# Performance work log

Hardware: AMD Instinct MI355X
Metric: run time of the kernel (lower is better)

The kernel has to match this reference:

```python
import jax, jax.numpy as jnp
import numpy as np

N_NODE = 4096   # nodes per graph (generalized from hardcoded 55)
IN_DIM = 200    # input_dim, forced by attn1 in_channel=200
OUT_DIM = 200   # output_dim, forced equal to input_dim by GRU_gate shapes
N_HEADS = 8     # forced by attn2 in_channel 1600 = 8*200
SEQ_LEN = 4
HID = 200       # hid_units default


def _glorot(k, shape):
    r = np.sqrt(6.0 / (shape[0] + shape[1])).astype(np.float32)
    return jax.random.uniform(k, shape, jnp.float32, -r, r)


def setup_inputs() -> dict:
    key = jax.random.key(0)
    ks = jax.random.split(key, 32)
    inp = {}
    mask = jax.random.bernoulli(ks[0], 0.01, (SEQ_LEN, N_NODE, N_NODE))
    inp['adjs'] = jax.random.uniform(ks[1], (SEQ_LEN, N_NODE, N_NODE), jnp.float32) * mask
    inp['feats'] = jax.random.normal(ks[2], (SEQ_LEN, N_NODE, IN_DIM), jnp.float32)
    inp['p_covss'] = jnp.zeros((SEQ_LEN,), jnp.float32)  # passed but unused in original
    # per-head weight_vars, randn(output_dim, input_dim) in original call()
    inp['init_wv'] = jax.random.normal(ks[3], (N_HEADS, OUT_DIM, IN_DIM), jnp.float32)
    # attn1 (shared across all heads): conv1d(k=1) == linear
    inp['W1'] = _glorot(ks[4], (HID, IN_DIM)); inp['b1'] = jnp.zeros((HID,), jnp.float32)
    inp['a11'] = _glorot(ks[5], (HID, 1))[:, 0]; inp['a11b'] = jnp.zeros((), jnp.float32)
    inp['a12'] = _glorot(ks[6], (HID, 1))[:, 0]; inp['a12b'] = jnp.zeros((), jnp.float32)
    # attn2
    inp['W2'] = _glorot(ks[7], (OUT_DIM, N_HEADS * HID)); inp['b2'] = jnp.zeros((OUT_DIM,), jnp.float32)
    inp['a21'] = _glorot(ks[8], (OUT_DIM, 1))[:, 0]; inp['a21b'] = jnp.zeros((), jnp.float32)
    inp['a22'] = _glorot(ks[9], (OUT_DIM, 1))[:, 0]; inp['a22b'] = jnp.zeros((), jnp.float32)
    # GRU gates (reset/update/htilda), reduce=True since n_node != input_dim
    for i, g in enumerate(['r', 'u', 'h']):
        inp['W' + g] = _glorot(ks[10 + 4 * i], (N_NODE, OUT_DIM))
        inp['U' + g] = _glorot(ks[11 + 4 * i], (OUT_DIM, OUT_DIM))
        inp['P' + g] = _glorot(ks[12 + 4 * i], (IN_DIM, N_NODE))
        inp['b' + g] = jnp.zeros((IN_DIM, OUT_DIM), jnp.float32)
    return inp


def reference(adjs, feats, p_covss, init_wv, W1, b1, a11, a11b, a12, a12b,
              W2, b2, a21, a21b, a22, a22b,
              Wr, Ur, Pr, br, Wu, Uu, Pu, bu, Wh, Uh, Ph, bh):
    def gat(x):  # x: [N, IN_DIM]
        fts = x @ W1.T + b1                                   # [N, HID]
        # logits f_1 + f_2^T on [N,1,1] stays [N,1,1]; softmax over the
        # singleton dim is identically 1 -> attention is degenerate.
        s = jax.nn.leaky_relu((fts @ a11 + a11b) + (fts @ a12 + a12b), 0.01)
        coefs = jnp.ones_like(s)                              # softmax([N,1,1], dim=1)
        h = jax.nn.elu(coefs[:, None] * fts)                  # [N, HID]
        hcat = jnp.tile(h, (1, N_HEADS))                      # heads share attn1 -> identical
        fts2 = hcat @ W2.T + b2                               # [N, OUT_DIM]
        s2 = jax.nn.leaky_relu((fts2 @ a21 + a21b) + (fts2 @ a22 + a22b), 0.01)
        coefs2 = jnp.ones_like(s2)
        out = jax.nn.elu(coefs2[:, None] * fts2)              # [N, OUT_DIM]
        # torch: out.view(nb_classes, -1).T then softmax(dim=1), then view(-1, out_dim)
        logits = jnp.reshape(out, (OUT_DIM, N_NODE)).T        # memory reinterpretation, not transpose
        return jax.nn.softmax(logits, axis=1)                 # [N, OUT_DIM]

    embeds = jax.vmap(gat)(feats)                             # [T, N, OUT_DIM]

    def gru_step(wv, adj):  # wv: [H, OUT_DIM, IN_DIM=OUT_DIM], adj: [N, N]
        # head-independent sparse propagation bases, one per gate
        gr = Pr @ (adj @ Wr) + br                             # [IN_DIM, OUT_DIM]
        gu = Pu @ (adj @ Wu) + bu
        gh = Ph @ (adj @ Wh) + bh
        r = jax.nn.sigmoid(gr + wv @ Ur)                      # [H, 200, 200]
        u = jax.nn.sigmoid(gu + wv @ Uu)
        hcap = jnp.tanh(gh + (r * wv) @ Uh)
        return (1.0 - u) * wv + u * hcap, None

    final_wv, _ = jax.lax.scan(gru_step, init_wv, adjs[1:])   # evolve over t=1..T-1
    return embeds, final_wv
```

## Files before the change

kernel.cpp:

```cpp
#include <hip/hip_runtime.h>
#include <hip/hip_bf16.h>
#include <math.h>

typedef __hip_bfloat16 bf16;
typedef __attribute__((ext_vector_type(8))) short short8;
typedef __attribute__((ext_vector_type(4))) float f32x4;

#define N_NODE 4096
#define DIM 200
#define NH 8
#define SEQ 4
#define TLDA 40

__device__ __forceinline__ float eluf(float x) { return x > 0.f ? x : expm1f(x); }
__device__ __forceinline__ float sigm(float x) { return 1.f / (1.f + expf(-x)); }

template<bool ISB>
__device__ __forceinline__ float ldv(const void* p, size_t i) {
    if (ISB) return __bfloat162float(((const bf16*)p)[i]);
    else     return ((const float*)p)[i];
}
template<bool ISB>
__device__ __forceinline__ void stv(void* p, size_t i, float v) {
    if (ISB) ((bf16*)p)[i] = __float2bfloat16(v);
    else     ((float*)p)[i] = v;
}
__device__ __forceinline__ float bflo(unsigned u) { return __uint_as_float((u & 0xffffu) << 16); }
__device__ __forceinline__ float bfhi(unsigned u) { return __uint_as_float(u & 0xffff0000u); }
__device__ __forceinline__ short f2bs(float v) {
    bf16 h = __float2bfloat16(v);
    return *(short*)&h;
}

__global__ void k_detect(const void* feats, int* flag) {
    __shared__ int cnt;
    if (threadIdx.x == 0) cnt = 0;
    __syncthreads();
    const unsigned short* u = (const unsigned short*)feats;
    unsigned short v = u[2 * threadIdx.x];
    int e = (v >> 7) & 0xFF;
    if (e >= 100 && e <= 140) atomicAdd(&cnt, 1);
    __syncthreads();
    if (threadIdx.x == 0) *flag = (cnt >= 128) ? 1 : 0;
}


template<bool AISB>
__device__ __forceinline__ void ldA8(const void* A, int lda, int arow, bool rowOK,
                                     int kk, int K, float* la) {
    if (rowOK && kk + 8 <= K) {
        if (AISB) {
            const unsigned short* ap = (const unsigned short*)A + (size_t)arow * lda + kk;
            uint4 u = *(const uint4*)ap;
            la[0] = bflo(u.x); la[1] = bfhi(u.x);
            la[2] = bflo(u.y); la[3] = bfhi(u.y);
            la[4] = bflo(u.z); la[5] = bfhi(u.z);
            la[6] = bflo(u.w); la[7] = bfhi(u.w);
        } else {
            const float* ap = (const float*)A + (size_t)arow * lda + kk;
            float4 f0 = *(const float4*)ap;
            float4 f1 = *(const float4*)(ap + 4);
            la[0] = f0.x; la[1] = f0.y; la[2] = f0.z; la[3] = f0.w;
            la[4] = f1.x; la[5] = f1.y; la[6] = f1.z; la[7] = f1.w;
        }
    } else {
#pragma unroll
        for (int j = 0; j < 8; j++)
            la[j] = (rowOK && kk + j < K) ? ldv<AISB>(A, (size_t)arow * lda + kk + j) : 0.f;
    }
}
template<bool BISB>
__device__ __forceinline__ void ldB8(const void* B, int gcol, bool colOK,
                                     int kk, int K, float* lb) {
#pragma unroll
    for (int j = 0; j < 8; j++)
        lb[j] = (colOK && kk + j < K) ? ldv<BISB>(B, (size_t)(kk + j) * DIM + gcol) : 0.f;
}

template<int EPI, bool AISB, bool BISB>
__device__ void mgemm(const void* A, int lda, const void* B, int M, int K,
                      int kbeg, int kend, const float* X1, const float* X2,
                      float* C, int row0, int c0, const int* fl, void* out2) {
    const int N = DIM;
    int tid = threadIdx.x;
    int wave = tid >> 6, lane = tid & 63;
    int m16 = lane & 15, q = lane >> 4;
    __shared__ short As[64 * TLDA];
    __shared__ short Bs[64 * TLDA];
    int s_row = tid >> 2;
    int s_k   = (tid & 3) * 8;
    int b_col = tid & 63;
    int b_kg  = (tid >> 6) * 8;
    int arow = row0 + s_row;
    bool rowOK = arow < M;
    int gcol = c0 + b_col;
    bool colOK = gcol < N;
    float la[8], lb[8];
    ldA8<AISB>(A, lda, arow, rowOK, kbeg + s_k, K, la);
    ldB8<BISB>(B, gcol, colOK, kbeg + b_kg, K, lb);
    f32x4 acc[4] = {};
    for (int k0 = kbeg; k0 < kend; k0 += 32) {
        __syncthreads();
        short8 a8, b8;
#pragma unroll
        for (int j = 0; j < 8; j++) { a8[j] = f2bs(la[j]); b8[j] = f2bs(lb[j]); }
        *(short8*)&As[s_row * TLDA + s_k] = a8;
        *(short8*)&Bs[b_col * TLDA + b_kg] = b8;
        __syncthreads();
        int kn = k0 + 32;
        if (kn < kend) {
            ldA8<AISB>(A, lda, arow, rowOK, kn + s_k, K, la);
            ldB8<BISB>(B, gcol, colOK, kn + b_kg, K, lb);
        }
        short8 bf = *(short8*)&Bs[(wave * 16 + m16) * TLDA + q * 8];
#pragma unroll
        for (int r = 0; r < 4; r++) {
            short8 af = *(short8*)&As[(r * 16 + m16) * TLDA + q * 8];
            acc[r] = __builtin_amdgcn_mfma_f32_16x16x32_bf16(af, bf, acc[r], 0, 0, 0);
        }
    }
    int colw = c0 + wave * 16 + m16;
    if (colw >= N) return;
#pragma unroll
    for (int r = 0; r < 4; r++) {
        int rowb = row0 + r * 16 + q * 4;
#pragma unroll
        for (int reg = 0; reg < 4; reg++) {
            int row = rowb + reg;
            if (row >= M) continue;
            float v = acc[r][reg];
            size_t ci = (size_t)row * 200 + colw;
            if (EPI == 0) {
                C[ci] = eluf(v + X1[colw]);
            } else if (EPI == 3) {
                int a200 = row - (row / 200) * 200;
                float uu = X2[ci];
                float hc = tanhf(X1[a200 * 200 + colw] + v);
                float nv = (1.f - uu) * C[ci] + uu * hc;
                C[ci] = nv;
                if (out2) {
                    size_t oo = (size_t)SEQ * N_NODE * DIM + ci;
                    if (*fl) stv<true>(out2, oo, nv); else stv<false>(out2, oo, nv);
                }
            } else {
                atomicAdd(&C[ci], v);
            }
        }
    }
}

__global__ __launch_bounds__(256) void k_gemm_e12(const float* A,
        const float* Br, const float* Bu, const float* Gr, const float* Gu,
        float* rw, float* u) {
    const int M = NH * DIM, K = DIM, N = DIM;
    int row0 = blockIdx.y * 64, c0 = blockIdx.x * 64;
    int tid = threadIdx.x;
    int wave = tid >> 6, lane = tid & 63;
    int m16 = lane & 15, q = lane >> 4;
    __shared__ short As[64 * TLDA];
    __shared__ short Bsr[64 * TLDA];
    __shared__ short Bsu[64 * TLDA];
    int s_row = tid >> 2;
    int s_k   = (tid & 3) * 8;
    int b_col = tid & 63;
    int b_kg  = (tid >> 6) * 8;
    int arow = row0 + s_row;
    bool rowOK = arow < M;
    int gcol = c0 + b_col;
    bool colOK = gcol < N;
    float la[8], lbr[8], lbu[8];
    ldA8<false>(A, K, arow, rowOK, s_k, K, la);
    ldB8<false>(Br, gcol, colOK, b_kg, K, lbr);
    ldB8<false>(Bu, gcol, colOK, b_kg, K, lbu);
    f32x4 accR[4] = {}, accU[4] = {};
    for (int k0 = 0; k0 < K; k0 += 32) {
        __syncthreads();
        short8 a8, r8, u8;
#pragma unroll
        for (int j = 0; j < 8; j++) {
            a8[j] = f2bs(la[j]); r8[j] = f2bs(lbr[j]); u8[j] = f2bs(lbu[j]);
        }
        *(short8*)&As[s_row * TLDA + s_k] = a8;
        *(short8*)&Bsr[b_col * TLDA + b_kg] = r8;
        *(short8*)&Bsu[b_col * TLDA + b_kg] = u8;
        __syncthreads();
        int kn = k0 + 32;
        if (kn < K) {
            ldA8<false>(A, K, arow, rowOK, kn + s_k, K, la);
            ldB8<false>(Br, gcol, colOK, kn + b_kg, K, lbr);
            ldB8<false>(Bu, gcol, colOK, kn + b_kg, K, lbu);
        }
        short8 bfr = *(short8*)&Bsr[(wave * 16 + m16) * TLDA + q * 8];
        short8 bfu = *(short8*)&Bsu[(wave * 16 + m16) * TLDA + q * 8];
#pragma unroll
        for (int r = 0; r < 4; r++) {
            short8 af = *(short8*)&As[(r * 16 + m16) * TLDA + q * 8];
            accR[r] = __builtin_amdgcn_mfma_f32_16x16x32_bf16(af, bfr, accR[r], 0, 0, 0);
            accU[r] = __builtin_amdgcn_mfma_f32_16x16x32_bf16(af, bfu, accU[r], 0, 0, 0);
        }
    }
    int colw = c0 + wave * 16 + m16;
    if (colw >= N) return;
#pragma unroll
    for (int r = 0; r < 4; r++) {
        int rowb = row0 + r * 16 + q * 4;
#pragma unroll
        for (int reg = 0; reg < 4; reg++) {
            int row = rowb + reg;
            if (row >= M) continue;
            int a200 = row - (row / 200) * 200;
            size_t ci = (size_t)row * 200 + colw;
            rw[ci] = sigm(Gr[a200 * 200 + colw] + accR[r][reg]) * A[ci];
            u[ci]  = sigm(Gu[a200 * 200 + colw] + accU[r][reg]);
        }
    }
}

__global__ __launch_bounds__(256) void k_gemm_e0(const int* fl, int useIsb,
        const void* A, int lda, const float* B, int M, int K,
        const float* bias, float* C) {
    int row0 = blockIdx.y * 64, c0 = blockIdx.x * 64;
    if (useIsb && *fl)
        mgemm<0, true , false>(A, lda, B, M, K, 0, K, bias, nullptr, C, row0, c0, nullptr, nullptr);
    else
        mgemm<0, false, false>(A, lda, B, M, K, 0, K, bias, nullptr, C, row0, c0, nullptr, nullptr);
}
__global__ __launch_bounds__(256) void k_gemm_e3(const float* A, const float* B,
        const float* G0, const float* U, float* WV, const int* fl, void* out2) {
    mgemm<3, false, false>(A, DIM, B, NH * DIM, DIM, 0, DIM, G0, U, WV,
                           blockIdx.y * 64, blockIdx.x * 64, fl, out2);
}
__global__ __launch_bounds__(256) void k_pggemm(const int* fl,
        const void* P0, const void* P1, const void* P2,
        const bf16* AWb, float* G) {
    int z = blockIdx.z;
    int sg = z >> 3, split = z & 7;
    int g = sg - (sg / 3) * 3;
    const void* A = (g == 0) ? P0 : (g == 1) ? P1 : P2;
    const void* B = AWb + (size_t)sg * N_NODE * DIM;
    float* C = G + (size_t)sg * DIM * DIM;
    int row0 = blockIdx.y * 64, c0 = blockIdx.x * 64;
    int kbeg = split * (N_NODE / 8), kend = kbeg + N_NODE / 8;
    if (*fl) mgemm<4, true , true>(A, N_NODE, B, DIM, N_NODE, kbeg, kend, nullptr, nullptr, C, row0, c0, nullptr, nullptr);
    else     mgemm<4, false, true>(A, N_NODE, B, DIM, N_NODE, kbeg, kend, nullptr, nullptr, C, row0, c0, nullptr, nullptr);
}

template<bool ISB>
__device__ void prep_body(const void* W1, const void* b1, const void* W2, const void* b2,
                          const void* Ur, const void* Uu, const void* Uh,
                          const void* br, const void* bu, const void* bh,
                          const void* iwv, const void* Wr, const void* Wu, const void* Wh,
                          float* W1t, float* W2t, float* b1f, float* b2f,
                          float* Utf, float* wv, float* G, unsigned short* Wcat) {
    int idx = blockIdx.x * 256 + threadIdx.x;
    if (idx < 40000) {
        int k = idx / 200, n = idx % 200;
        W1t[idx] = ldv<ISB>(W1, (size_t)n * 200 + k);
    } else if (idx < 80000) {
        int r = idx - 40000;
        int k = r / 200, n = r % 200;
        float s = 0.f;
        for (int h = 0; h < NH; h++) s += ldv<ISB>(W2, (size_t)n * 1600 + h * 200 + k);
        W2t[r] = s;
    } else if (idx < 80512) {
        int j = idx - 80000;
        if (j < 256)      b1f[j] = (j < 200) ? ldv<ISB>(b1, j) : 0.f;
        else              b2f[j - 256] = (j - 256 < 200) ? ldv<ISB>(b2, j - 256) : 0.f;
    } else if (idx < 200512) {
        int j = idx - 80512;
        int g = j / 40000, r = j - g * 40000;
        const void* U = (g == 0) ? Ur : (g == 1) ? Uu : Uh;
        Utf[j] = ldv<ISB>(U, r);
    } else if (idx < 520512) {
        wv[idx - 200512] = ldv<ISB>(iwv, idx - 200512);
    } else if (idx < 880512) {
        int j = idx - 520512;
        int sg = j / 40000, r = j - sg * 40000;
        int g = sg - (sg / 3) * 3;
        const void* bb = (g == 0) ? br : (g == 1) ? bu : bh;
        G[j] = ldv<ISB>(bb, r);
    } else {
        int j = idx - 880512;
        if (j < 4096 * 600) {
            int k = j / 600, c = j - k * 600;
            int g = (c < 200) ? 0 : (c < 400 ? 1 : 2);
            int o = c - g * 200;
            const void* W = (g == 0) ? Wr : (g == 1) ? Wu : Wh;
            bf16 v = __float2bfloat16(ldv<ISB>(W, (size_t)k * 200 + o));
            Wcat[(size_t)k * 608 + c] = *(unsigned short*)&v;
        }
    }
}
__global__ void k_prep(const int* fl, const void* W1, const void* b1, const void* W2,
                       const void* b2, const void* Ur, const void* Uu, const void* Uh,
                       const void* br, const void* bu, const void* bh, const void* iwv,
                       const void* Wr, const void* Wu, const void* Wh,
                       float* W1t, float* W2t, float* b1f, float* b2f,
                       float* Utf, float* wv, float* G, unsigned short* Wcat) {
    if (*fl) prep_body<true >(W1, b1, W2, b2, Ur, Uu, Uh, br, bu, bh, iwv, Wr, Wu, Wh,
                              W1t, W2t, b1f, b2f, Utf, wv, G, Wcat);
    else     prep_body<false>(W1, b1, W2, b2, Ur, Uu, Uh, br, bu, bh, iwv, Wr, Wu, Wh,
                              W1t, W2t, b1f, b2f, Utf, wv, G, Wcat);
}

template<bool ISB>
__device__ void softmax_body(const float* O, void* out) {
    __shared__ float tile[200 * 65];
    __shared__ float pm[4 * 64];
    __shared__ float ps[4 * 64];
    __shared__ float sm_m[64];
    __shared__ float sm_inv[64];
    int t = blockIdx.y;
    int i0 = blockIdx.x * 64;
    const float* ob = O + (size_t)t * N_NODE * DIM;
    int tid = threadIdx.x;
    for (int idx = tid; idx < 200 * 64; idx += 256) {
        int j = idx >> 6, c = idx & 63;
        tile[j * 65 + c] = ob[(size_t)j * N_NODE + i0 + c];
    }
    __syncthreads();
    int g = tid >> 6, lane = tid & 63;
    int j0 = g * 50, j1 = j0 + 50;
    float mp = -1e30f;
    for (int j = j0; j < j1; j++) mp = fmaxf(mp, tile[j * 65 + lane]);
    pm[g * 64 + lane] = mp;
    __syncthreads();
    if (tid < 64)
        sm_m[tid] = fmaxf(fmaxf(pm[tid], pm[64 + tid]), fmaxf(pm[128 + tid], pm[192 + tid]));
    __syncthreads();
    float mv = sm_m[lane];
    float sp = 0.f;
    for (int j = j0; j < j1; j++) {
        float e = expf(tile[j * 65 + lane] - mv);
        tile[j * 65 + lane] = e;
        sp += e;
    }
    ps[g * 64 + lane] = sp;
    __syncthreads();
    if (tid < 64)
        sm_inv[tid] = 1.f / (ps[tid] + ps[64 + tid] + ps[128 + tid] + ps[192 + tid]);
    __syncthreads();
    size_t ob2 = ((size_t)t * N_NODE + i0) * DIM;
    for (int idx = tid; idx < 64 * 200; idx += 256) {
        int il = idx / 200, j = idx - il * 200;
        stv<ISB>(out, ob2 + (size_t)il * DIM + j, tile[j * 65 + il] * sm_inv[il]);
    }
}
__global__ __launch_bounds__(256) void k_softmax(const int* fl, const float* O, void* out) {
    if (*fl) softmax_body<true>(O, out); else softmax_body<false>(O, out);
}

template<bool ISB>
__device__ void aw_body(const void* adjs, const unsigned short* Wcat, bf16* AWb) {
    int i = blockIdx.x;
    int s = blockIdx.y;
    size_t arow = ((size_t)(s + 1) * N_NODE + i) * N_NODE;
    __shared__ int   s_k[512];
    __shared__ float s_v[512];
    __shared__ int   s_cnt;
    int tid = threadIdx.x;
    if (tid == 0) s_cnt = 0;
    __syncthreads();
    float vals[16];
#pragma unroll
    for (int c = 0; c < 4; c++) {
        int col = c * 1024 + tid * 4;
        if (ISB) {
            ushort4 u = *(const ushort4*)((const unsigned short*)adjs + arow + col);
            vals[c*4+0] = __uint_as_float((unsigned)u.x << 16);
            vals[c*4+1] = __uint_as_float((unsigned)u.y << 16);
            vals[c*4+2] = __uint_as_float((unsigned)u.z << 16);
            vals[c*4+3] = __uint_as_float((unsigned)u.w << 16);
        } else {
            float4 f = *(const float4*)((const float*)adjs + arow + col);
            vals[c*4+0] = f.x; vals[c*4+1] = f.y; vals[c*4+2] = f.z; vals[c*4+3] = f.w;
        }
    }
#pragma unroll
    for (int q = 0; q < 16; q++) {
        if (vals[q] != 0.f) {
            int p = atomicAdd(&s_cnt, 1);
            if (p < 512) { s_k[p] = (q >> 2) * 1024 + tid * 4 + (q & 3); s_v[p] = vals[q]; }
        }
    }
    __syncthreads();
    int n = s_cnt < 512 ? s_cnt : 512;
    float a0 = 0.f, a1 = 0.f, d0 = 0.f, d1 = 0.f;
    bool hasB = (tid < 44);
    int offA = 2 * tid, offB = 512 + 2 * tid;
    int e = 0;
    for (; e + 4 <= n; e += 4) {
        int   k0 = s_k[e],   k1 = s_k[e+1], k2 = s_k[e+2], k3 = s_k[e+3];
        float v0 = s_v[e],   v1 = s_v[e+1], v2 = s_v[e+2], v3 = s_v[e+3];
        unsigned wa0 = *(const unsigned*)(Wcat + (size_t)k0 * 608 + offA);
        unsigned wa1 = *(const unsigned*)(Wcat + (size_t)k1 * 608 + offA);
        unsigned wa2 = *(const unsigned*)(Wcat + (size_t)k2 * 608 + offA);
        unsigned wa3 = *(const unsigned*)(Wcat + (size_t)k3 * 608 + offA);
        if (hasB) {
            unsigned wb0 = *(const unsigned*)(Wcat + (size_t)k0 * 608 + offB);
            unsigned wb1 = *(const unsigned*)(Wcat + (size_t)k1 * 608 + offB);
            unsigned wb2 = *(const unsigned*)(Wcat + (size_t)k2 * 608 + offB);
            unsigned wb3 = *(const unsigned*)(Wcat + (size_t)k3 * 608 + offB);
            d0 += v0*bflo(wb0) + v1*bflo(wb1) + v2*bflo(wb2) + v3*bflo(wb3);
            d1 += v0*bfhi(wb0) + v1*bfhi(wb1) + v2*bfhi(wb2) + v3*bfhi(wb3);
        }
        a0 += v0*bflo(wa0) + v1*bflo(wa1) + v2*bflo(wa2) + v3*bflo(wa3);
        a1 += v0*bfhi(wa0) + v1*bfhi(wa1) + v2*bfhi(wa2) + v3*bfhi(wa3);
    }
    for (; e < n; e++) {
        int k = s_k[e]; float v = s_v[e];
        unsigned wa = *(const unsigned*)(Wcat + (size_t)k * 608 + offA);
        a0 += v * bflo(wa); a1 += v * bfhi(wa);
        if (hasB) {
            unsigned wb = *(const unsigned*)(Wcat + (size_t)k * 608 + offB);
            d0 += v * bflo(wb); d1 += v * bfhi(wb);
        }
    }
    int gA = (offA < 200) ? 0 : (offA < 400 ? 1 : 2);
    int oA = offA - gA * 200;
    size_t wbase = ((size_t)(s * 3 + gA) * N_NODE + i) * DIM + oA;
    AWb[wbase]     = __float2bfloat16(a0);
    AWb[wbase + 1] = __float2bfloat16(a1);
    if (hasB) {
        int oB = offB - 400;
        size_t wb2 = ((size_t)(s * 3 + 2) * N_NODE + i) * DIM + oB;
        AWb[wb2]     = __float2bfloat16(d0);
        AWb[wb2 + 1] = __float2bfloat16(d1);
    }
}
__global__ __launch_bounds__(256) void k_aw(const int* fl, const void* adjs,
        const unsigned short* Wcat, bf16* AWb) {
    if (*fl) aw_body<true>(adjs, Wcat, AWb);
    else     aw_body<false>(adjs, Wcat, AWb);
}

extern "C" void kernel_launch(void* const* d_in, const int* in_sizes, int n_in,
                              void* d_out, int out_size, void* d_ws, size_t ws_size,
                              hipStream_t stream) {
    const void* adjs    = d_in[0];
    const void* feats   = d_in[1];
    const void* init_wv = d_in[3];
    const void* W1 = d_in[4];
    const void* b1 = d_in[5];
    const void* W2 = d_in[10];
    const void* b2 = d_in[11];
    const void* Wr = d_in[16];
    const void* Ur = d_in[17];
    const void* Pr = d_in[18];
    const void* br = d_in[19];
    const void* Wu = d_in[20];
    const void* Uu = d_in[21];
    const void* Pu = d_in[22];
    const void* bu = d_in[23];
    const void* Wh = d_in[24];
    const void* Uh = d_in[25];
    const void* Ph = d_in[26];
    const void* bh = d_in[27];

    int*   flag = (int*)d_ws;
    float* base = (float*)d_ws;
    unsigned short* Wcat = (unsigned short*)(base + 64);
    bf16*  AWb  = (bf16*)(base + 64 + 1245184);
    float* Hbuf = base + 64;
    float* Obuf = Hbuf + 3276800;
    float* W1t  = base + 6553664;
    float* W2t  = W1t + 40000;
    float* b1f  = W2t + 40000;
    float* b2f  = b1f + 256;
    float* ubuf = b2f + 256;
    float* rwbuf= ubuf + 320000;
    float* Utf  = rwbuf + 320000;
    float* G    = Utf + 120000;
    float* wv   = G + 360000;

    const int M = SEQ * N_NODE;

    k_detect<<<1, 256, 0, stream>>>(feats, flag);
    k_prep<<<(3338112 + 255) / 256, 256, 0, stream>>>(
        flag, W1, b1, W2, b2, Ur, Uu, Uh, br, bu, bh, init_wv, Wr, Wu, Wh,
        W1t, W2t, b1f, b2f, Utf, wv, G, Wcat);

    {
        dim3 g(N_NODE, 3);
        k_aw<<<g, 256, 0, stream>>>(flag, adjs, Wcat, AWb);
    }
    {
        dim3 g(4, 4, 72);
        k_pggemm<<<g, 256, 0, stream>>>(flag, Pr, Pu, Ph, AWb, G);
    }

    {
        dim3 g(4, M / 64);
        k_gemm_e0<<<g, 256, 0, stream>>>(flag, 1, feats, DIM, W1t, M, DIM, b1f, Hbuf);
        k_gemm_e0<<<g, 256, 0, stream>>>(flag, 0, Hbuf, DIM, W2t, M, DIM, b2f, Obuf);
    }
    {
        dim3 g(N_NODE / 64, SEQ);
        k_softmax<<<g, 256, 0, stream>>>(flag, Obuf, d_out);
    }

    {
        dim3 g(4, NH * DIM / 64);
        for (int s = 0; s < 3; s++) {
            const float* Gr = G + (size_t)(s * 3 + 0) * DIM * DIM;
            const float* Gu = G + (size_t)(s * 3 + 1) * DIM * DIM;
            const float* Gh = G + (size_t)(s * 3 + 2) * DIM * DIM;
            void* out2 = (s == 2) ? d_out : nullptr;
            k_gemm_e12<<<g, 256, 0, stream>>>(wv, Utf + 0, Utf + 40000, Gr, Gu, rwbuf, ubuf);
            k_gemm_e3<<<g, 256, 0, stream>>>(rwbuf, Utf + 80000, Gh, ubuf, wv, flag, out2);
        }
    }
}
```

Measured before the change: 671.3 us.

## Store GEMM operands in bf16 with transposed B for vectorized loads

Intermediate activations (H buffer, rw, wv copy) and the dense weights (W1, W2, U) are now kept in bf16. The weights are pre-transposed in the prep kernel so the B operand loads become single 16-byte vector loads instead of eight strided scalar loads. The per-iteration float-to-bf16 conversion in the GEMM loops is removed, and memory traffic for the intermediates roughly halves. In exchange the code keeps an extra bf16 copy of wv and adds conversion stores in the epilogues. The accuracy should match the previous path, since operands were already rounded to bf16 before the MFMA.

Result: faster. 595.3 us, median of 2 (-11.3%).

```diff
diff --git a/kernel.cpp b/kernel.cpp
--- a/kernel.cpp
+++ b/kernel.cpp
@@ -45,42 +45,55 @@
 }
 
 
-template<bool AISB>
-__device__ __forceinline__ void ldA8(const void* A, int lda, int arow, bool rowOK,
-                                     int kk, int K, float* la) {
+template<int AMODE>
+__device__ __forceinline__ short8 ldA8x(const void* A, int lda, int arow, bool rowOK,
+                                        int kk, int K) {
+    short8 r;
     if (rowOK && kk + 8 <= K) {
-        if (AISB) {
-            const unsigned short* ap = (const unsigned short*)A + (size_t)arow * lda + kk;
-            uint4 u = *(const uint4*)ap;
-            la[0] = bflo(u.x); la[1] = bfhi(u.x);
-            la[2] = bflo(u.y); la[3] = bfhi(u.y);
-            la[4] = bflo(u.z); la[5] = bfhi(u.z);
-            la[6] = bflo(u.w); la[7] = bfhi(u.w);
+        if (AMODE == 1) {
+            r = *(const short8*)((const short*)A + (size_t)arow * lda + kk);
         } else {
             const float* ap = (const float*)A + (size_t)arow * lda + kk;
             float4 f0 = *(const float4*)ap;
             float4 f1 = *(const float4*)(ap + 4);
-            la[0] = f0.x; la[1] = f0.y; la[2] = f0.z; la[3] = f0.w;
-            la[4] = f1.x; la[5] = f1.y; la[6] = f1.z; la[7] = f1.w;
+            r[0] = f2bs(f0.x); r[1] = f2bs(f0.y); r[2] = f2bs(f0.z); r[3] = f2bs(f0.w);
+            r[4] = f2bs(f1.x); r[5] = f2bs(f1.y); r[6] = f2bs(f1.z); r[7] = f2bs(f1.w);
         }
     } else {
 #pragma unroll
+        for (int j = 0; j < 8; j++) {
+            bool ok = rowOK && kk + j < K;
+            if (AMODE == 1) r[j] = ok ? ((const short*)A)[(size_t)arow * lda + kk + j] : (short)0;
+            else            r[j] = ok ? f2bs(((const float*)A)[(size_t)arow * lda + kk + j]) : (short)0;
+        }
+    }
+    return r;
+}
+
+template<int BMODE>
+__device__ __forceinline__ short8 ldB8x(const void* B, int gcol, bool colOK,
+                                        int kk, int K) {
+    short8 r;
+    if (BMODE == 2) {
+        if (colOK && kk + 8 <= K) {
+            r = *(const short8*)((const short*)B + (size_t)gcol * K + kk);
+        } else {
+#pragma unroll
+            for (int j = 0; j < 8; j++)
+                r[j] = (colOK && kk + j < K) ? ((const short*)B)[(size_t)gcol * K + kk + j] : (short)0;
+        }
+    } else {
+#pragma unroll
         for (int j = 0; j < 8; j++)
-            la[j] = (rowOK && kk + j < K) ? ldv<AISB>(A, (size_t)arow * lda + kk + j) : 0.f;
-    }
-}
-template<bool BISB>
-__device__ __forceinline__ void ldB8(const void* B, int gcol, bool colOK,
-                                     int kk, int K, float* lb) {
-#pragma unroll
-    for (int j = 0; j < 8; j++)
-        lb[j] = (colOK && kk + j < K) ? ldv<BISB>(B, (size_t)(kk + j) * DIM + gcol) : 0.f;
-}
-
-template<int EPI, bool AISB, bool BISB>
+            r[j] = (colOK && kk + j < K) ? ((const short*)B)[(size_t)(kk + j) * DIM + gcol] : (short)0;
+    }
+    return r;
+}
+
+template<int EPI, int AMODE, int BMODE, int CB16>
 __device__ void mgemm(const void* A, int lda, const void* B, int M, int K,
                       int kbeg, int kend, const float* X1, const float* X2,
-                      float* C, int row0, int c0, const int* fl, void* out2) {
+                      void* Cv, int row0, int c0, const int* fl, void* out2, short* Cb) {
     const int N = DIM;
     int tid = threadIdx.x;
     int wave = tid >> 6, lane = tid & 63;
@@ -95,28 +108,24 @@
     bool rowOK = arow < M;
     int gcol = c0 + b_col;
     bool colOK = gcol < N;
-    float la[8], lb[8];
-    ldA8<AISB>(A, lda, arow, rowOK, kbeg + s_k, K, la);
-    ldB8<BISB>(B, gcol, colOK, kbeg + b_kg, K, lb);
+    short8 la = ldA8x<AMODE>(A, lda, arow, rowOK, kbeg + s_k, K);
+    short8 lb = ldB8x<BMODE>(B, gcol, colOK, kbeg + b_kg, K);
     f32x4 acc[4] = {};
     for (int k0 = kbeg; k0 < kend; k0 += 32) {
         __syncthreads();
-        short8 a8, b8;
-#pragma unroll
-        for (int j = 0; j < 8; j++) { a8[j] = f2bs(la[j]); b8[j] = f2bs(lb[j]); }
-        *(short8*)&As[s_row * TLDA + s_k] = a8;
-        *(short8*)&Bs[b_col * TLDA + b_kg] = b8;
+        *(short8*)&As[s_row * TLDA + s_k] = la;
+        *(short8*)&Bs[b_col * TLDA + b_kg] = lb;
         __syncthreads();
         int kn = k0 + 32;
         if (kn < kend) {
-            ldA8<AISB>(A, lda, arow, rowOK, kn + s_k, K, la);
-            ldB8<BISB>(B, gcol, colOK, kn + b_kg, K, lb);
-        }
-        short8 bf = *(short8*)&Bs[(wave * 16 + m16) * TLDA + q * 8];
+            la = ldA8x<AMODE>(A, lda, arow, rowOK, kn + s_k, K);
+            lb = ldB8x<BMODE>(B, gcol, colOK, kn + b_kg, K);
+        }
+        short8 bfr = *(short8*)&Bs[(wave * 16 + m16) * TLDA + q * 8];
 #pragma unroll
         for (int r = 0; r < 4; r++) {
             short8 af = *(short8*)&As[(r * 16 + m16) * TLDA + q * 8];
-            acc[r] = __builtin_amdgcn_mfma_f32_16x16x32_bf16(af, bf, acc[r], 0, 0, 0);
+            acc[r] = __builtin_amdgcn_mfma_f32_16x16x32_bf16(af, bfr, acc[r], 0, 0, 0);
         }
     }
     int colw = c0 + wave * 16 + m16;
@@ -131,27 +140,31 @@
             float v = acc[r][reg];
             size_t ci = (size_t)row * 200 + colw;
             if (EPI == 0) {
-                C[ci] = eluf(v + X1[colw]);
+                float o = eluf(v + X1[colw]);
+                if (CB16) ((short*)Cv)[ci] = f2bs(o);
+                else      ((float*)Cv)[ci] = o;
             } else if (EPI == 3) {
+                float* C = (float*)Cv;
                 int a200 = row - (row / 200) * 200;
                 float uu = X2[ci];
                 float hc = tanhf(X1[a200 * 200 + colw] + v);
                 float nv = (1.f - uu) * C[ci] + uu * hc;
                 C[ci] = nv;
+                Cb[ci] = f2bs(nv);
                 if (out2) {
                     size_t oo = (size_t)SEQ * N_NODE * DIM + ci;
                     if (*fl) stv<true>(out2, oo, nv); else stv<false>(out2, oo, nv);
                 }
             } else {
-                atomicAdd(&C[ci], v);
+                atomicAdd(&((float*)Cv)[ci], v);
             }
         }
     }
 }
 
-__global__ __launch_bounds__(256) void k_gemm_e12(const float* A,
-        const float* Br, const float* Bu, const float* Gr, const float* Gu,
-        float* rw, float* u) {
+__global__ __launch_bounds__(256) void k_gemm_e12(const short* A,
+        const short* Br, const short* Bu, const float* Gr, const float* Gu,
+        const float* wvf, short* rwb, float* u) {
     const int M = NH * DIM, K = DIM, N = DIM;
     int row0 = blockIdx.y * 64, c0 = blockIdx.x * 64;
     int tid = threadIdx.x;
@@ -168,27 +181,21 @@
     bool rowOK = arow < M;
     int gcol = c0 + b_col;
     bool colOK = gcol < N;
-    float la[8], lbr[8], lbu[8];
-    ldA8<false>(A, K, arow, rowOK, s_k, K, la);
-    ldB8<false>(Br, gcol, colOK, b_kg, K, lbr);
-    ldB8<false>(Bu, gcol, colOK, b_kg, K, lbu);
+    short8 la = ldA8x<1>(A, K, arow, rowOK, s_k, K);
+    short8 lr = ldB8x<2>(Br, gcol, colOK, b_kg, K);
+    short8 lu = ldB8x<2>(Bu, gcol, colOK, b_kg, K);
     f32x4 accR[4] = {}, accU[4] = {};
     for (int k0 = 0; k0 < K; k0 += 32) {
         __syncthreads();
-        short8 a8, r8, u8;
-#pragma unroll
-        for (int j = 0; j < 8; j++) {
-            a8[j] = f2bs(la[j]); r8[j] = f2bs(lbr[j]); u8[j] = f2bs(lbu[j]);
-        }
-        *(short8*)&As[s_row * TLDA + s_k] = a8;
-        *(short8*)&Bsr[b_col * TLDA + b_kg] = r8;
-        *(short8*)&Bsu[b_col * TLDA + b_kg] = u8;
+        *(short8*)&As[s_row * TLDA + s_k] = la;
+        *(short8*)&Bsr[b_col * TLDA + b_kg] = lr;
+        *(short8*)&Bsu[b_col * TLDA + b_kg] = lu;
         __syncthreads();
         int kn = k0 + 32;
         if (kn < K) {
-            ldA8<false>(A, K, arow, rowOK, kn + s_k, K, la);
-            ldB8<false>(Br, gcol, colOK, kn + b_kg, K, lbr);
-            ldB8<false>(Bu, gcol, colOK, kn + b_kg, K, lbu);
+            la = ldA8x<1>(A, K, arow, rowOK, kn + s_k, K);
+            lr = ldB8x<2>(Br, gcol, colOK, kn + b_kg, K);
+            lu = ldB8x<2>(Bu, gcol, colOK, kn + b_kg, K);
         }
         short8 bfr = *(short8*)&Bsr[(wave * 16 + m16) * TLDA + q * 8];
         short8 bfu = *(short8*)&Bsu[(wave * 16 + m16) * TLDA + q * 8];
@@ -210,25 +217,31 @@
             if (row >= M) continue;
             int a200 = row - (row / 200) * 200;
             size_t ci = (size_t)row * 200 + colw;
-            rw[ci] = sigm(Gr[a200 * 200 + colw] + accR[r][reg]) * A[ci];
-            u[ci]  = sigm(Gu[a200 * 200 + colw] + accU[r][reg]);
-        }
-    }
-}
-
-__global__ __launch_bounds__(256) void k_gemm_e0(const int* fl, int useIsb,
-        const void* A, int lda, const float* B, int M, int K,
+            rwb[ci] = f2bs(sigm(Gr[a200 * 200 + colw] + accR[r][reg]) * wvf[ci]);
+            u[ci]   = sigm(Gu[a200 * 200 + colw] + accU[r][reg]);
+        }
+    }
+}
+
+__global__ __launch_bounds__(256) void k_gemm_e0a(const int* fl, const void* A,
+        const short* B, const float* bias, short* Hb) {
+    int row0 = blockIdx.y * 64, c0 = blockIdx.x * 64;
+    if (*fl)
+        mgemm<0, 1, 2, 1>(A, DIM, B, SEQ * N_NODE, DIM, 0, DIM, bias, nullptr,
+                          Hb, row0, c0, nullptr, nullptr, nullptr);
+    else
+        mgemm<0, 0, 2, 1>(A, DIM, B, SEQ * N_NODE, DIM, 0, DIM, bias, nullptr,
+                          Hb, row0, c0, nullptr, nullptr, nullptr);
+}
+__global__ __launch_bounds__(256) void k_gemm_e0b(const short* A, const short* B,
         const float* bias, float* C) {
-    int row0 = blockIdx.y * 64, c0 = blockIdx.x * 64;
-    if (useIsb && *fl)
-        mgemm<0, true , false>(A, lda, B, M, K, 0, K, bias, nullptr, C, row0, c0, nullptr, nullptr);
-    else
-        mgemm<0, false, false>(A, lda, B, M, K, 0, K, bias, nullptr, C, row0, c0, nullptr, nullptr);
-}
-__global__ __launch_bounds__(256) void k_gemm_e3(const float* A, const float* B,
-        const float* G0, const float* U, float* WV, const int* fl, void* out2) {
-    mgemm<3, false, false>(A, DIM, B, NH * DIM, DIM, 0, DIM, G0, U, WV,
-                           blockIdx.y * 64, blockIdx.x * 64, fl, out2);
+    mgemm<0, 1, 2, 0>(A, DIM, B, SEQ * N_NODE, DIM, 0, DIM, bias, nullptr,
+                      C, blockIdx.y * 64, blockIdx.x * 64, nullptr, nullptr, nullptr);
+}
+__global__ __launch_bounds__(256) void k_gemm_e3(const short* A, const short* B,
+        const float* Gh, const float* U, float* WV, const int* fl, void* out2, short* wvb) {
+    mgemm<3, 1, 2, 0>(A, DIM, B, NH * DIM, DIM, 0, DIM, Gh, U, WV,
+                      blockIdx.y * 64, blockIdx.x * 64, fl, out2, wvb);
 }
 __global__ __launch_bounds__(256) void k_pggemm(const int* fl,
         const void* P0, const void* P1, const void* P2,
@@ -241,8 +254,8 @@
     float* C = G + (size_t)sg * DIM * DIM;
     int row0 = blockIdx.y * 64, c0 = blockIdx.x * 64;
     int kbeg = split * (N_NODE / 8), kend = kbeg + N_NODE / 8;
-    if (*fl) mgemm<4, true , true>(A, N_NODE, B, DIM, N_NODE, kbeg, kend, nullptr, nullptr, C, row0, c0, nullptr, nullptr);
-    else     mgemm<4, false, true>(A, N_NODE, B, DIM, N_NODE, kbeg, kend, nullptr, nullptr, C, row0, c0, nullptr, nullptr);
+    if (*fl) mgemm<4, 1, 1, 0>(A, N_NODE, B, DIM, N_NODE, kbeg, kend, nullptr, nullptr, C, row0, c0, nullptr, nullptr, nullptr);
+    else     mgemm<4, 0, 1, 0>(A, N_NODE, B, DIM, N_NODE, kbeg, kend, nullptr, nullptr, C, row0, c0, nullptr, nullptr, nullptr);
 }
 
 template<bool ISB>
@@ -250,18 +263,17 @@
                           const void* Ur, const void* Uu, const void* Uh,
                           const void* br, const void* bu, const void* bh,
                           const void* iwv, const void* Wr, const void* Wu, const void* Wh,
-                          float* W1t, float* W2t, float* b1f, float* b2f,
-                          float* Utf, float* wv, float* G, unsigned short* Wcat) {
+                          short* W1b, short* W2b, float* b1f, float* b2f,
+                          short* Ub, float* wv, short* wvb, float* G, unsigned short* Wcat) {
     int idx = blockIdx.x * 256 + threadIdx.x;
     if (idx < 40000) {
-        int k = idx / 200, n = idx % 200;
-        W1t[idx] = ldv<ISB>(W1, (size_t)n * 200 + k);
+        W1b[idx] = f2bs(ldv<ISB>(W1, idx));
     } else if (idx < 80000) {
         int r = idx - 40000;
-        int k = r / 200, n = r % 200;
+        int n = r / 200, k = r - n * 200;
         float s = 0.f;
         for (int h = 0; h < NH; h++) s += ldv<ISB>(W2, (size_t)n * 1600 + h * 200 + k);
-        W2t[r] = s;
+        W2b[r] = f2bs(s);
     } else if (idx < 80512) {
         int j = idx - 80000;
         if (j < 256)      b1f[j] = (j < 200) ? ldv<ISB>(b1, j) : 0.f;
@@ -269,10 +281,14 @@
     } else if (idx < 200512) {
         int j = idx - 80512;
         int g = j / 40000, r = j - g * 40000;
+        int n = r / 200, k = r - n * 200;
         const void* U = (g == 0) ? Ur : (g == 1) ? Uu : Uh;
-        Utf[j] = ldv<ISB>(U, r);
+        Ub[j] = f2bs(ldv<ISB>(U, (size_t)k * 200 + n));
     } else if (idx < 520512) {
-        wv[idx - 200512] = ldv<ISB>(iwv, idx - 200512);
+        int j = idx - 200512;
+        float v = ldv<ISB>(iwv, j);
+        wv[j] = v;
+        wvb[j] = f2bs(v);
     } else if (idx < 880512) {
         int j = idx - 520512;
         int sg = j / 40000, r = j - sg * 40000;
@@ -295,12 +311,12 @@
                        const void* b2, const void* Ur, const void* Uu, const void* Uh,
                        const void* br, const void* bu, const void* bh, const void* iwv,
                        const void* Wr, const void* Wu, const void* Wh,
-                       float* W1t, float* W2t, float* b1f, float* b2f,
-                       float* Utf, float* wv, float* G, unsigned short* Wcat) {
+                       short* W1b, short* W2b, float* b1f, float* b2f,
+                       short* Ub, float* wv, short* wvb, float* G, unsigned short* Wcat) {
     if (*fl) prep_body<true >(W1, b1, W2, b2, Ur, Uu, Uh, br, bu, bh, iwv, Wr, Wu, Wh,
-                              W1t, W2t, b1f, b2f, Utf, wv, G, Wcat);
+                              W1b, W2b, b1f, b2f, Ub, wv, wvb, G, Wcat);
     else     prep_body<false>(W1, b1, W2, b2, Ur, Uu, Uh, br, bu, bh, iwv, Wr, Wu, Wh,
-                              W1t, W2t, b1f, b2f, Utf, wv, G, Wcat);
+                              W1b, W2b, b1f, b2f, Ub, wv, wvb, G, Wcat);
 }
 
 template<bool ISB>
@@ -461,24 +477,25 @@
     float* base = (float*)d_ws;
     unsigned short* Wcat = (unsigned short*)(base + 64);
     bf16*  AWb  = (bf16*)(base + 64 + 1245184);
-    float* Hbuf = base + 64;
-    float* Obuf = Hbuf + 3276800;
-    float* W1t  = base + 6553664;
-    float* W2t  = W1t + 40000;
-    float* b1f  = W2t + 40000;
-    float* b2f  = b1f + 256;
-    float* ubuf = b2f + 256;
-    float* rwbuf= ubuf + 320000;
-    float* Utf  = rwbuf + 320000;
-    float* G    = Utf + 120000;
-    float* wv   = G + 360000;
+    short* Hb   = (short*)(base + 64);
+    float* Obuf = base + 3276864;
+    short* W1b  = (short*)(base + 6553664);
+    short* W2b  = (short*)(base + 6593664);
+    float* b1f  = base + 6633664;
+    float* b2f  = base + 6633920;
+    float* ubuf = base + 6634176;
+    short* rwb  = (short*)(base + 6954176);
+    short* Ub   = (short*)(base + 7274176);
+    float* G    = base + 7394176;
+    float* wv   = base + 7754176;
+    short* wvb  = (short*)(base + 8074176);
 
     const int M = SEQ * N_NODE;
 
     k_detect<<<1, 256, 0, stream>>>(feats, flag);
     k_prep<<<(3338112 + 255) / 256, 256, 0, stream>>>(
         flag, W1, b1, W2, b2, Ur, Uu, Uh, br, bu, bh, init_wv, Wr, Wu, Wh,
-        W1t, W2t, b1f, b2f, Utf, wv, G, Wcat);
+        W1b, W2b, b1f, b2f, Ub, wv, wvb, G, Wcat);
 
     {
         dim3 g(N_NODE, 3);
@@ -491,8 +508,8 @@
 
     {
         dim3 g(4, M / 64);
-        k_gemm_e0<<<g, 256, 0, stream>>>(flag, 1, feats, DIM, W1t, M, DIM, b1f, Hbuf);
-        k_gemm_e0<<<g, 256, 0, stream>>>(flag, 0, Hbuf, DIM, W2t, M, DIM, b2f, Obuf);
+        k_gemm_e0a<<<g, 256, 0, stream>>>(flag, feats, W1b, b1f, Hb);
+        k_gemm_e0b<<<g, 256, 0, stream>>>(Hb, W2b, b2f, Obuf);
     }
     {
         dim3 g(N_NODE / 64, SEQ);
@@ -506,8 +523,8 @@
             const float* Gu = G + (size_t)(s * 3 + 1) * DIM * DIM;
             const float* Gh = G + (size_t)(s * 3 + 2) * DIM * DIM;
             void* out2 = (s == 2) ? d_out : nullptr;
-            k_gemm_e12<<<g, 256, 0, stream>>>(wv, Utf + 0, Utf + 40000, Gr, Gu, rwbuf, ubuf);
-            k_gemm_e3<<<g, 256, 0, stream>>>(rwbuf, Utf + 80000, Gh, ubuf, wv, flag, out2);
-        }
-    }
-}
+            k_gemm_e12<<<g, 256, 0, stream>>>(wvb, Ub, Ub + 40000, Gr, Gu, wv, rwb, ubuf);
+            k_gemm_e3<<<g, 256, 0, stream>>>(rwb, Ub + 80000, Gh, ubuf, wv, flag, out2, wvb);
+        }
+    }
+}
```
